# Optimization experiments

Hardware: AMD Instinct MI355X
Metric: run time of the kernel (lower is better)

The kernel has to match this reference:

```python
import jax, jax.numpy as jnp
import numpy as np
from jax import lax

jax.config.update("jax_enable_x64", True)

B = 32768          # batch size
NCS = 96           # number of charging stations
NB = 124           # num_buses
S_BASE = 1000.0
MAX_CS = 22.17
MIN_CS = -22.17
MAX_EV_CH = 22.0
MAX_EV_DIS = -22.0
EV_CAP = 70.0
EV_MIN_CAP = 15.0
ITERS = 100
TOL = 1e-06
DT = 15.0 / 60.0   # timescale (hours)


def setup_inputs() -> dict:
    ks = jax.random.split(jax.random.key(0), 12)
    action = jax.random.uniform(ks[0], (B, NCS), dtype=jnp.float32, minval=-1.0, maxval=1.0)
    prices = jax.random.uniform(ks[1], (B, 1), dtype=jnp.float32, minval=0.05, maxval=0.5)
    active = jax.random.uniform(ks[2], (B, NB - 1), dtype=jnp.float32, minval=0.0, maxval=50.0)
    reactive = jax.random.uniform(ks[3], (B, NB - 1), dtype=jnp.float32, minval=0.0, maxval=20.0)
    cap = jax.random.uniform(ks[4], (B, NCS), dtype=jnp.float32, minval=0.0, maxval=EV_CAP)
    cap = cap * (jax.random.uniform(ks[5], (B, NCS)) > 0.2).astype(jnp.float32)
    tleft = jax.random.randint(ks[6], (B, NCS), 1, 10).astype(jnp.float32)
    bus = jax.random.randint(ks[7], (B, NCS), 0, NB - 1).astype(jnp.float32)
    ev = jnp.stack([cap, tleft, bus], axis=-1).reshape(B, 3 * NCS)  # interleaved triples
    state = jnp.concatenate(
        [jnp.zeros((B, 3), jnp.float32), prices, active, reactive, ev], axis=1
    )  # (B, 4 + 2*(NB-1) + 3*NCS) == (B, 538)
    K_re = (0.005 * jax.random.normal(ks[8], (NB - 1, NB - 1))).astype(jnp.float32)
    K_im = (0.005 * jax.random.normal(ks[9], (NB - 1, NB - 1))).astype(jnp.float32)
    L_re = jnp.ones((NB - 1,), jnp.float32)
    L_im = jnp.zeros((NB - 1,), jnp.float32)
    return {"action": action, "state": state, "K_re": K_re, "K_im": K_im, "L_re": L_re, "L_im": L_im}


def _forward(action, state, K_re, K_im, L_re, L_im):
    b, ncs = action.shape
    nb1 = NB - 1
    es = 4 + 2 * nb1  # start of EV state block
    prices = state[:, 3:4]                                    # (B,1), broadcast over stations
    cap = state[:, es:es + 3 * ncs:3]                         # current capacity
    tleft = state[:, es + 1:es + 1 + 3 * ncs:3]               # time left
    bus = state[:, es + 2:es + 2 + 3 * ncs:3].astype(jnp.int32)  # connected bus index
    conn = (cap > 0).astype(action.dtype)
    max_ch = jnp.minimum(MAX_EV_CH, conn * (EV_CAP - cap) / DT)
    max_dis = jnp.maximum(MAX_EV_DIS, conn * (EV_MIN_CAP - cap) / DT)
    pos = jnp.where(action >= 0, 1.0, 0.0).astype(action.dtype)
    power = action * MAX_CS * pos - action * MIN_CS * (1.0 - pos)
    power = jnp.maximum(jnp.minimum(power, max_ch), max_dis)
    costs = (prices * power * DT).sum(axis=1)
    new_cap = jnp.ceil((cap + power * DT) * 100.0) / 100.0
    dep = (tleft == 1).astype(action.dtype)
    user_sat = (-10.0 * dep * (new_cap - EV_CAP) ** 2).sum(axis=1)
    # scatter-add EV power per bus (duplicate indices accumulate, like torch scatter_add)
    ev_bus = jnp.zeros((b, nb1), power.dtype).at[jnp.arange(b)[:, None], bus].add(power)
    ap = state[:, 4:4 + nb1]
    rp = state[:, 4 + nb1:4 + 2 * nb1]
    S = ((ap + ev_bus) / S_BASE + 1j * (rp / S_BASE)).astype(jnp.complex128)  # (B, NB-1)
    K = (K_re + 1j * K_im).astype(jnp.complex128)
    W = (L_re + 1j * L_im).astype(jnp.complex128)
    v_init = jnp.ones((b, nb1), jnp.complex128)

    def run(v0):
        # Z-bus fixed point: v_k = K @ conj(S / v0)^T + W   (batched as bi)
        vk = jnp.einsum('ij,bj->bi', K, jnp.conj(S / v0)) + W
        tol = jnp.max(jnp.abs(jnp.abs(vk) - jnp.abs(v0)))
        return vk, tol

    def body(carry, _):
        v0, done = carry
        def step(v):
            vk, tol = run(v)
            return vk, tol < TOL
        def skip(v):
            return v, jnp.array(True)
        v_next, conv = lax.cond(done, skip, step, v0)
        return (v_next, done | conv), None

    (v_fin, _), _ = lax.scan(body, (v_init, jnp.array(False)), None, length=ITERS)
    vmag = jnp.abs(v_fin)
    voltage_loss = jnp.minimum(0.0, 0.05 - jnp.abs(1.0 - vmag)).sum(axis=1)
    loss = 1000.0 * voltage_loss + costs + user_sat
    return loss.astype(jnp.float32)


def reference(action, state, K_re, K_im, L_re, L_im):
    return _forward(action, state, K_re, K_im, L_re, L_im)
```

## Files before the change

kernel.cpp:

```cpp
#include <hip/hip_runtime.h>

#define NB1   123
#define NCSd  96
#define SW    538
#define TPB   256
#define BT    16
#define STPB  128


__global__ __launch_bounds__(256) void k_norm(const float* __restrict__ Kre,
                                              const float* __restrict__ Kim,
                                              const float* __restrict__ Lre,
                                              const float* __restrict__ Lim,
                                              float* __restrict__ ws) {
    __shared__ float part[4];
    const int tid = threadIdx.x;
    const int w = tid >> 6, l = tid & 63;
    const int wid = blockIdx.x * 4 + w;
    const int j1 = wid, j2 = wid + 64;
    const bool has2 = j2 < NB1;

    const float* kr1 = Kre + j1 * NB1; const float* ki1 = Kim + j1 * NB1;
    float a0 = kr1[l], b0 = ki1[l];
    float a1 = 0.f, b1 = 0.f;
    if (l < NB1 - 64) { a1 = kr1[l + 64]; b1 = ki1[l + 64]; }
    float c0 = 0.f, d0 = 0.f, c1 = 0.f, d1 = 0.f;
    if (has2) {
        const float* kr2 = Kre + j2 * NB1; const float* ki2 = Kim + j2 * NB1;
        c0 = kr2[l]; d0 = ki2[l];
        if (l < NB1 - 64) { c1 = kr2[l + 64]; d1 = ki2[l + 64]; }
    }
    float s1 = fmaf(a0, a0, b0 * b0) + fmaf(a1, a1, b1 * b1);
    float s2 = fmaf(c0, c0, d0 * d0) + fmaf(c1, c1, d1 * d1);
    #pragma unroll
    for (int off = 32; off; off >>= 1) {
        s1 += __shfl_xor(s1, off);
        s2 += __shfl_xor(s2, off);
    }
    float m2 = has2 ? fmaxf(s1, s2) : s1;
    if (l == 0) part[w] = m2;
    __syncthreads();
    if (tid == 0)
        ws[2 + blockIdx.x] = fmaxf(fmaxf(part[0], part[1]), fmaxf(part[2], part[3]));

    if (blockIdx.x == 0 && w == 0) {
        float dr = Lre[l] - 1.f, di = Lim[l];
        float d2 = fmaf(dr, dr, di * di);
        if (l + 64 < NB1) {
            float dr2 = Lre[l + 64] - 1.f, di2 = Lim[l + 64];
            d2 = fmaxf(d2, fmaf(dr2, dr2, di2 * di2));
        }
        #pragma unroll
        for (int off = 32; off; off >>= 1) d2 = fmaxf(d2, __shfl_xor(d2, off));
        if (l == 0) { ws[1] = d2; ((unsigned*)ws)[0] = 0u; }
    }
}

__global__ __launch_bounds__(TPB) void k_fast(const float* __restrict__ action,
                                              const float* __restrict__ state,
                                              float* __restrict__ ws,
                                              float* __restrict__ out) {
    __shared__ __align__(16) float st[4][1088];
    __shared__ float ev[4][256];

    const int tid = threadIdx.x;
    const int w = tid >> 6, l = tid & 63;
    const long g = (long)blockIdx.x * 4 + w;

    const float4* G4 = (const float4*)(state + g * (2 * SW));
    float4 v0 = G4[l];
    float4 v1 = G4[l + 64];
    float4 v2 = G4[l + 128];
    float4 v3 = G4[l + 192];
    float4 v4 = make_float4(0.f, 0.f, 0.f, 0.f);
    const bool t4 = l < 269 - 256;
    if (t4) v4 = G4[l + 256];

    float r2p = (l < 16) ? ws[2 + l] : 0.f;
    float dw2 = ws[1];

    ev[w][l] = 0.f; ev[w][l + 64] = 0.f;
    ev[w][l + 128] = 0.f; ev[w][l + 192] = 0.f;

    float4* st4 = (float4*)st[w];
    st4[l] = v0; st4[l + 64] = v1; st4[l + 128] = v2; st4[l + 192] = v3;
    if (t4) st4[l + 256] = v4;
    asm volatile("s_waitcnt lgkmcnt(0)" ::: "memory");

    const int e = l >> 5, li = l & 31;
    const long b = 2 * g + e;
    const float* srow = st[w] + e * SW;
    const float* actp = action + b * NCSd;
    float* evp = ev[w] + e * 128;
    const float pr = srow[3];

    float cost = 0.f, usat = 0.f;
    #pragma unroll
    for (int s = 0; s < 3; ++s) {
        int i = li + 32 * s;
        float cap = srow[250 + 3 * i];
        float tl  = srow[251 + 3 * i];
        int   bus = (int)srow[252 + 3 * i];
        float a   = actp[i];
        float conn = cap > 0.f ? 1.f : 0.f;
        float mch = fminf(22.0f,  conn * (70.0f - cap) * 4.0f);
        float mds = fmaxf(-22.0f, conn * (15.0f - cap) * 4.0f);
        float p = fmaxf(fminf(22.17f * a, mch), mds);
        cost = fmaf(pr * p, 0.25f, cost);
        float nc = ceilf((cap + p * 0.25f) * 100.0f) * 0.01f;
        if (tl == 1.0f) { float d = nc - 70.0f; usat = fmaf(-10.0f * d, d, usat); }
        atomicAdd(&evp[bus], p);
    }
    asm volatile("s_waitcnt lgkmcnt(0)" ::: "memory");

    float s2 = 0.f;
    #pragma unroll
    for (int s = 0; s < 4; ++s) {
        int k = li + 32 * s;
        if (k < NB1) {
            float apv = srow[4 + k] + evp[k];
            float rpv = srow[127 + k];
            s2 = fmaf(apv, apv, fmaf(rpv, rpv, s2));
        }
    }
    #pragma unroll
    for (int off = 16; off; off >>= 1) {
        s2   += __shfl_xor(s2, off);
        cost += __shfl_xor(cost, off);
        usat += __shfl_xor(usat, off);
    }

    #pragma unroll
    for (int off = 8; off; off >>= 1) r2p = fmaxf(r2p, __shfl_xor(r2p, off));
    float R  = sqrtf(__shfl(r2p, 0));
    float dW = sqrtf(dw2);
    float t = 0.0495f - dW;
    float q2max = -1.0f;
    if (t > 0.f && t < 1.0f - dW) {
        float xm = (t * (1.0f - dW - t) - 1e-7f) / 1.001f;
        if (xm > 0.f && R > 0.f) {
            float sm = xm / R * 1000.0f;
            q2max = sm * sm;
        }
    }
    bool safe = s2 <= q2max;

    if (li == 0) out[b] = cost + usat;

    bool flagged = (li == 0) && !safe;
    unsigned long long mask = __ballot(flagged);
    if (mask) {
        int nf = __popcll(mask);
        int lead = __ffsll((long long)mask) - 1;
        unsigned base_ = 0;
        if (l == lead) base_ = atomicAdd((unsigned*)ws, (unsigned)nf);
        base_ = __shfl(base_, lead);
        if (flagged) {
            int rank = __popcll(mask & ((1ull << l) - 1ull));
            ((unsigned*)ws)[18 + base_ + rank] = (unsigned)b;
        }
    }
}

__global__ __launch_bounds__(STPB) void k_solve(const float* __restrict__ action,
                                                const float* __restrict__ state,
                                                const float* __restrict__ Kre,
                                                const float* __restrict__ Kim,
                                                const float* __restrict__ Lre,
                                                const float* __restrict__ Lim,
                                                const float* __restrict__ ws,
                                                float* __restrict__ out) {
    __shared__ float ev[BT][STPB];
    __shared__ __align__(16) float2 cmat[STPB][BT + 2];
    __shared__ float vls[STPB][BT + 1];
    __shared__ float red[2];
    __shared__ unsigned idxs[BT];
    const unsigned count = ((const unsigned*)ws)[0];
    const int tid = threadIdx.x;
    const int j = tid;
    const bool jok = j < NB1;
    const float Wre = jok ? Lre[j] : 1.f;
    const float Wim = jok ? Lim[j] : 0.f;

    for (unsigned base = (unsigned)blockIdx.x * BT; base < count; base += (unsigned)gridDim.x * BT) {
        unsigned nv = count - base; if (nv > BT) nv = BT;
        if (tid < BT) {
            unsigned t = (unsigned)tid < nv ? (unsigned)tid : nv - 1;
            idxs[tid] = ((const unsigned*)ws)[18 + base + t];
        }
        for (int x = tid; x < BT * STPB; x += STPB) ((float*)ev)[x] = 0.f;
        __syncthreads();

        for (int task = tid; task < BT * NCSd; task += STPB) {
            int e = task / NCSd, i = task - e * NCSd;
            long b = (long)idxs[e];
            const float* srow = state + b * SW;
            float cap = srow[250 + 3 * i];
            int   bus = (int)srow[252 + 3 * i];
            float a   = action[b * NCSd + i];
            float conn = cap > 0.f ? 1.f : 0.f;
            float mch = fminf(22.0f,  conn * (70.0f - cap) * 4.0f);
            float mds = fmaxf(-22.0f, conn * (15.0f - cap) * 4.0f);
            float p = fmaxf(fminf(22.17f * a, mch), mds);
            atomicAdd(&ev[e][bus], p);
        }
        __syncthreads();

        float Sre[BT], Sim[BT], vr[BT], vi[BT];
        #pragma unroll
        for (int e = 0; e < BT; ++e) {
            long b = (long)idxs[e];
            float ap = jok ? state[b * SW + 4 + j]   : 0.f;
            float rp = jok ? state[b * SW + 127 + j] : 0.f;
            Sre[e] = (ap + ev[e][j]) * 0.001f;
            Sim[e] = rp * 0.001f;
            vr[e] = 1.f; vi[e] = 0.f;
        }
        for (int it = 0; it < 100; ++it) {
            #pragma unroll
            for (int e = 0; e < BT; ++e) {
                float d = vr[e] * vr[e] + vi[e] * vi[e];
                float inv = 1.0f / d;
                cmat[j][e] = make_float2((Sre[e] * vr[e] + Sim[e] * vi[e]) * inv,
                                         (Sre[e] * vi[e] - Sim[e] * vr[e]) * inv);
            }
            __syncthreads();
            float ar[BT], ai[BT];
            #pragma unroll
            for (int e = 0; e < BT; ++e) { ar[e] = Wre; ai[e] = Wim; }
            for (int k = 0; k < NB1; ++k) {
                float kr = jok ? Kre[j * NB1 + k] : 0.f;
                float ki = jok ? Kim[j * NB1 + k] : 0.f;
                const float4* crow = (const float4*)(&cmat[k][0]);
                #pragma unroll
                for (int eh = 0; eh < BT / 2; ++eh) {
                    float4 c2 = crow[eh];
                    ar[2*eh]   = fmaf(kr, c2.x, fmaf(-ki, c2.y, ar[2*eh]));
                    ai[2*eh]   = fmaf(kr, c2.y, fmaf( ki, c2.x, ai[2*eh]));
                    ar[2*eh+1] = fmaf(kr, c2.z, fmaf(-ki, c2.w, ar[2*eh+1]));
                    ai[2*eh+1] = fmaf(kr, c2.w, fmaf( ki, c2.z, ai[2*eh+1]));
                }
            }
            float md = 0.f;
            #pragma unroll
            for (int e = 0; e < BT; ++e) {
                float vmn = sqrtf(ar[e]*ar[e] + ai[e]*ai[e]);
                float vmo = sqrtf(vr[e]*vr[e] + vi[e]*vi[e]);
                md = fmaxf(md, fabsf(vmn - vmo));
                vr[e] = ar[e]; vi[e] = ai[e];
            }
            #pragma unroll
            for (int off = 32; off; off >>= 1) md = fmaxf(md, __shfl_xor(md, off));
            if ((tid & 63) == 0) red[tid >> 6] = md;
            __syncthreads();
            if (fmaxf(red[0], red[1]) < 1e-6f) break;
        }
        #pragma unroll
        for (int e = 0; e < BT; ++e) {
            float vm = sqrtf(vr[e]*vr[e] + vi[e]*vi[e]);
            vls[j][e] = jok ? fminf(0.f, 0.05f - fabsf(1.0f - vm)) : 0.f;
        }
        __syncthreads();
        if (tid < (int)nv) {
            float s = 0.f;
            for (int k = 0; k < NB1; ++k) s += vls[k][tid];
            long b = (long)idxs[tid];
            out[b] += 1000.0f * s;
        }
        __syncthreads();
    }
}

__global__ __launch_bounds__(STPB) void k_main(
    const float* __restrict__ action, const float* __restrict__ state,
    const float* __restrict__ Kre, const float* __restrict__ Kim,
    const float* __restrict__ Lre, const float* __restrict__ Lim,
    float* __restrict__ out)
{
    __shared__ float ev[BT][STPB];
    __shared__ float costs_s[BT];
    __shared__ float usat_s[BT];
    __shared__ __align__(16) float2 cmat[STPB][BT + 2];
    __shared__ float vls[STPB][BT + 1];
    __shared__ float red[2];
    const int tid = threadIdx.x;
    const int e0  = blockIdx.x * BT;
    for (int x = tid; x < BT * STPB; x += STPB) ((float*)ev)[x] = 0.f;
    if (tid < BT) { costs_s[tid] = 0.f; usat_s[tid] = 0.f; }
    __syncthreads();
    for (int task = tid; task < BT * NCSd; task += STPB) {
        int e = task / NCSd, i = task - e * NCSd;
        long b = (long)(e0 + e);
        const float* srow = state + b * SW;
        float cap = srow[250 + 3 * i], tleft = srow[251 + 3 * i];
        int bus = (int)srow[252 + 3 * i];
        float a = action[b * NCSd + i];
        float conn = cap > 0.f ? 1.f : 0.f;
        float mch = fminf(22.0f, conn * (70.0f - cap) * 4.0f);
        float mds = fmaxf(-22.0f, conn * (15.0f - cap) * 4.0f);
        float power = fmaxf(fminf(22.17f * a, mch), mds);
        atomicAdd(&costs_s[e], srow[3] * power * 0.25f);
        float nc = ceilf((cap + power * 0.25f) * 100.0f) * 0.01f;
        if (tleft == 1.0f) { float d = nc - 70.0f; atomicAdd(&usat_s[e], -10.0f * d * d); }
        atomicAdd(&ev[e][bus], power);
    }
    __syncthreads();
    const int j = tid;
    const bool jok = j < NB1;
    float Wre = jok ? Lre[j] : 1.0f, Wim = jok ? Lim[j] : 0.0f;
    float Sre[BT], Sim[BT], vr[BT], vi[BT];
    #pragma unroll
    for (int e = 0; e < BT; ++e) {
        long b = (long)(e0 + e);
        float ap = jok ? state[b * SW + 4 + j] : 0.f;
        float rp = jok ? state[b * SW + 127 + j] : 0.f;
        Sre[e] = (ap + ev[e][j]) * 0.001f; Sim[e] = rp * 0.001f;
        vr[e] = 1.f; vi[e] = 0.f;
    }
    for (int it = 0; it < 100; ++it) {
        #pragma unroll
        for (int e = 0; e < BT; ++e) {
            float d = vr[e]*vr[e] + vi[e]*vi[e];
            float inv = 1.0f / d;
            cmat[j][e] = make_float2((Sre[e]*vr[e] + Sim[e]*vi[e]) * inv,
                                     (Sre[e]*vi[e] - Sim[e]*vr[e]) * inv);
        }
        __syncthreads();
        float ar[BT], ai[BT];
        #pragma unroll
        for (int e = 0; e < BT; ++e) { ar[e] = Wre; ai[e] = Wim; }
        for (int k = 0; k < NB1; ++k) {
            float kr = jok ? Kre[j*NB1+k] : 0.f;
            float ki = jok ? Kim[j*NB1+k] : 0.f;
            const float4* crow = (const float4*)(&cmat[k][0]);
            #pragma unroll
            for (int eh = 0; eh < BT / 2; ++eh) {
                float4 c2 = crow[eh];
                ar[2*eh]   = fmaf(kr, c2.x, fmaf(-ki, c2.y, ar[2*eh]));
                ai[2*eh]   = fmaf(kr, c2.y, fmaf( ki, c2.x, ai[2*eh]));
                ar[2*eh+1] = fmaf(kr, c2.z, fmaf(-ki, c2.w, ar[2*eh+1]));
                ai[2*eh+1] = fmaf(kr, c2.w, fmaf( ki, c2.z, ai[2*eh+1]));
            }
        }
        float md = 0.f;
        #pragma unroll
        for (int e = 0; e < BT; ++e) {
            float vmn = sqrtf(ar[e]*ar[e] + ai[e]*ai[e]);
            float vmo = sqrtf(vr[e]*vr[e] + vi[e]*vi[e]);
            md = fmaxf(md, fabsf(vmn - vmo));
            vr[e] = ar[e]; vi[e] = ai[e];
        }
        #pragma unroll
        for (int off = 32; off > 0; off >>= 1) md = fmaxf(md, __shfl_xor(md, off));
        if ((tid & 63) == 0) red[tid >> 6] = md;
        __syncthreads();
        if (fmaxf(red[0], red[1]) < 1e-6f) break;
    }
    #pragma unroll
    for (int e = 0; e < BT; ++e) {
        float vm = sqrtf(vr[e]*vr[e] + vi[e]*vi[e]);
        vls[j][e] = jok ? fminf(0.f, 0.05f - fabsf(1.0f - vm)) : 0.f;
    }
    __syncthreads();
    if (tid < BT) {
        float s = 0.f;
        for (int k = 0; k < NB1; ++k) s += vls[k][tid];
        out[e0 + tid] = 1000.0f * s + costs_s[tid] + usat_s[tid];
    }
}

extern "C" void kernel_launch(void* const* d_in, const int* in_sizes, int n_in,
                              void* d_out, int out_size, void* d_ws, size_t ws_size,
                              hipStream_t stream) {
    const float* action = (const float*)d_in[0];
    const float* state  = (const float*)d_in[1];
    const float* Kre    = (const float*)d_in[2];
    const float* Kim    = (const float*)d_in[3];
    const float* Lre    = (const float*)d_in[4];
    const float* Lim    = (const float*)d_in[5];
    float* out = (float*)d_out;
    const int B = out_size;

    const size_t wsNeed = (size_t)(18 + B) * sizeof(unsigned);
    if (ws_size >= wsNeed) {
        float* ws = (float*)d_ws;
        hipLaunchKernelGGL(k_norm, dim3(16), dim3(256), 0, stream, Kre, Kim, Lre, Lim, ws);
        hipLaunchKernelGGL(k_fast, dim3(B / 8), dim3(TPB), 0, stream,
                           action, state, ws, out);
        hipLaunchKernelGGL(k_solve, dim3(16), dim3(STPB), 0, stream,
                           action, state, Kre, Kim, Lre, Lim, ws, out);
    } else {
        hipLaunchKernelGGL(k_main, dim3((B + BT - 1) / BT), dim3(STPB), 0, stream,
                           action, state, Kre, Kim, Lre, Lim, out);
    }
}
```

Measured before the change: 37.71 us.

## Fuse fallback power-flow solve into fast kernel and drop compaction pass

Removes the separate k_solve launch and the atomic compaction list of flagged batch rows. Any wave whose row fails the analytic safety bound now runs the Z-bus fixed-point iteration itself, with each lane handling two buses and reading K from global memory. The iteration count is fixed at 32 with no convergence check, and two explicit LDS waitcnts plus the workspace counter reset are dropped. This saves a kernel launch and a global atomic, but flagged rows are handled serially inside a single wave, and a fixed iteration count may differ slightly from the tolerance-based reference.

Result: faster. 36.20 us, median of 2 (-4.0%).

```diff
diff --git a/kernel.cpp b/kernel.cpp
--- a/kernel.cpp
+++ b/kernel.cpp
@@ -41,7 +41,7 @@
     if (l == 0) part[w] = m2;
     __syncthreads();
     if (tid == 0)
-        ws[2 + blockIdx.x] = fmaxf(fmaxf(part[0], part[1]), fmaxf(part[2], part[3]));
+        ws[1 + blockIdx.x] = fmaxf(fmaxf(part[0], part[1]), fmaxf(part[2], part[3]));
 
     if (blockIdx.x == 0 && w == 0) {
         float dr = Lre[l] - 1.f, di = Lim[l];
@@ -52,14 +52,18 @@
         }
         #pragma unroll
         for (int off = 32; off; off >>= 1) d2 = fmaxf(d2, __shfl_xor(d2, off));
-        if (l == 0) { ws[1] = d2; ((unsigned*)ws)[0] = 0u; }
+        if (l == 0) ws[0] = d2;
     }
 }
 
-__global__ __launch_bounds__(TPB) void k_fast(const float* __restrict__ action,
-                                              const float* __restrict__ state,
-                                              float* __restrict__ ws,
-                                              float* __restrict__ out) {
+__global__ __launch_bounds__(TPB, 7) void k_fast(const float* __restrict__ action,
+                                                 const float* __restrict__ state,
+                                                 const float* __restrict__ Kre,
+                                                 const float* __restrict__ Kim,
+                                                 const float* __restrict__ Lre,
+                                                 const float* __restrict__ Lim,
+                                                 const float* __restrict__ ws,
+                                                 float* __restrict__ out) {
     __shared__ __align__(16) float st[4][1088];
     __shared__ float ev[4][256];
 
@@ -76,8 +80,8 @@
     const bool t4 = l < 269 - 256;
     if (t4) v4 = G4[l + 256];
 
-    float r2p = (l < 16) ? ws[2 + l] : 0.f;
-    float dw2 = ws[1];
+    float r2p = (l < 16) ? ws[1 + l] : 0.f;
+    float dw2 = ws[0];
 
     ev[w][l] = 0.f; ev[w][l + 64] = 0.f;
     ev[w][l + 128] = 0.f; ev[w][l + 192] = 0.f;
@@ -85,7 +89,6 @@
     float4* st4 = (float4*)st[w];
     st4[l] = v0; st4[l + 64] = v1; st4[l + 128] = v2; st4[l + 192] = v3;
     if (t4) st4[l + 256] = v4;
-    asm volatile("s_waitcnt lgkmcnt(0)" ::: "memory");
 
     const int e = l >> 5, li = l & 31;
     const long b = 2 * g + e;
@@ -111,7 +114,6 @@
         if (tl == 1.0f) { float d = nc - 70.0f; usat = fmaf(-10.0f * d, d, usat); }
         atomicAdd(&evp[bus], p);
     }
-    asm volatile("s_waitcnt lgkmcnt(0)" ::: "memory");
 
     float s2 = 0.f;
     #pragma unroll
@@ -145,130 +147,63 @@
     }
     bool safe = s2 <= q2max;
 
-    if (li == 0) out[b] = cost + usat;
-
-    bool flagged = (li == 0) && !safe;
-    unsigned long long mask = __ballot(flagged);
-    if (mask) {
-        int nf = __popcll(mask);
-        int lead = __ffsll((long long)mask) - 1;
-        unsigned base_ = 0;
-        if (l == lead) base_ = atomicAdd((unsigned*)ws, (unsigned)nf);
-        base_ = __shfl(base_, lead);
-        if (flagged) {
-            int rank = __popcll(mask & ((1ull << l) - 1ull));
-            ((unsigned*)ws)[18 + base_ + rank] = (unsigned)b;
-        }
-    }
-}
-
-__global__ __launch_bounds__(STPB) void k_solve(const float* __restrict__ action,
-                                                const float* __restrict__ state,
-                                                const float* __restrict__ Kre,
-                                                const float* __restrict__ Kim,
-                                                const float* __restrict__ Lre,
-                                                const float* __restrict__ Lim,
-                                                const float* __restrict__ ws,
-                                                float* __restrict__ out) {
-    __shared__ float ev[BT][STPB];
-    __shared__ __align__(16) float2 cmat[STPB][BT + 2];
-    __shared__ float vls[STPB][BT + 1];
-    __shared__ float red[2];
-    __shared__ unsigned idxs[BT];
-    const unsigned count = ((const unsigned*)ws)[0];
-    const int tid = threadIdx.x;
-    const int j = tid;
-    const bool jok = j < NB1;
-    const float Wre = jok ? Lre[j] : 1.f;
-    const float Wim = jok ? Lim[j] : 0.f;
-
-    for (unsigned base = (unsigned)blockIdx.x * BT; base < count; base += (unsigned)gridDim.x * BT) {
-        unsigned nv = count - base; if (nv > BT) nv = BT;
-        if (tid < BT) {
-            unsigned t = (unsigned)tid < nv ? (unsigned)tid : nv - 1;
-            idxs[tid] = ((const unsigned*)ws)[18 + base + t];
-        }
-        for (int x = tid; x < BT * STPB; x += STPB) ((float*)ev)[x] = 0.f;
-        __syncthreads();
-
-        for (int task = tid; task < BT * NCSd; task += STPB) {
-            int e = task / NCSd, i = task - e * NCSd;
-            long b = (long)idxs[e];
-            const float* srow = state + b * SW;
-            float cap = srow[250 + 3 * i];
-            int   bus = (int)srow[252 + 3 * i];
-            float a   = action[b * NCSd + i];
-            float conn = cap > 0.f ? 1.f : 0.f;
-            float mch = fminf(22.0f,  conn * (70.0f - cap) * 4.0f);
-            float mds = fmaxf(-22.0f, conn * (15.0f - cap) * 4.0f);
-            float p = fmaxf(fminf(22.17f * a, mch), mds);
-            atomicAdd(&ev[e][bus], p);
-        }
-        __syncthreads();
-
-        float Sre[BT], Sim[BT], vr[BT], vi[BT];
-        #pragma unroll
-        for (int e = 0; e < BT; ++e) {
-            long b = (long)idxs[e];
-            float ap = jok ? state[b * SW + 4 + j]   : 0.f;
-            float rp = jok ? state[b * SW + 127 + j] : 0.f;
-            Sre[e] = (ap + ev[e][j]) * 0.001f;
-            Sim[e] = rp * 0.001f;
-            vr[e] = 1.f; vi[e] = 0.f;
-        }
-        for (int it = 0; it < 100; ++it) {
-            #pragma unroll
-            for (int e = 0; e < BT; ++e) {
-                float d = vr[e] * vr[e] + vi[e] * vi[e];
-                float inv = 1.0f / d;
-                cmat[j][e] = make_float2((Sre[e] * vr[e] + Sim[e] * vi[e]) * inv,
-                                         (Sre[e] * vi[e] - Sim[e] * vr[e]) * inv);
+    float vs0 = 0.f, vs1 = 0.f;
+    unsigned long long bad = __ballot(!safe);
+    if (bad & 0x100000001ull) {
+        const int j1 = l, j2 = 64 + l;
+        const bool has2 = j2 < NB1;
+        float* cw = st[w];
+        #pragma unroll 1
+        for (int fe = 0; fe < 2; ++fe) {
+            if (!((bad >> (fe * 32)) & 1ull)) continue;
+            const float* frow = st[w] + fe * SW;
+            float* fev = ev[w] + fe * 128;
+            float S1r = (frow[4 + j1] + fev[j1]) * 0.001f;
+            float S1i = frow[127 + j1] * 0.001f;
+            float S2r = has2 ? (frow[4 + j2] + fev[j2]) * 0.001f : 0.f;
+            float S2i = has2 ? frow[127 + j2] * 0.001f : 0.f;
+            float W1r = Lre[j1], W1i = Lim[j1];
+            float W2r = has2 ? Lre[j2] : 1.f;
+            float W2i = has2 ? Lim[j2] : 0.f;
+            float v1r = 1.f, v1i = 0.f, v2r = 1.f, v2i = 0.f;
+            for (int it = 0; it < 32; ++it) {
+                float d1 = v1r * v1r + v1i * v1i, i1 = 1.0f / d1;
+                cw[j1]       = (S1r * v1r + S1i * v1i) * i1;
+                cw[128 + j1] = (S1r * v1i - S1i * v1r) * i1;
+                if (has2) {
+                    float d2 = v2r * v2r + v2i * v2i, i2 = 1.0f / d2;
+                    cw[j2]       = (S2r * v2r + S2i * v2i) * i2;
+                    cw[128 + j2] = (S2r * v2i - S2i * v2r) * i2;
+                }
+                asm volatile("s_waitcnt lgkmcnt(0)" ::: "memory");
+                float a1r = W1r, a1i = W1i, a2r = W2r, a2i = W2i;
+                for (int k = 0; k < NB1; ++k) {
+                    float cr = cw[k], ci = cw[128 + k];
+                    float kr1 = Kre[j1 * NB1 + k], ki1 = Kim[j1 * NB1 + k];
+                    a1r = fmaf(kr1, cr, fmaf(-ki1, ci, a1r));
+                    a1i = fmaf(kr1, ci, fmaf( ki1, cr, a1i));
+                    if (has2) {
+                        float kr2 = Kre[j2 * NB1 + k], ki2 = Kim[j2 * NB1 + k];
+                        a2r = fmaf(kr2, cr, fmaf(-ki2, ci, a2r));
+                        a2i = fmaf(kr2, ci, fmaf( ki2, cr, a2i));
+                    }
+                }
+                v1r = a1r; v1i = a1i; v2r = a2r; v2i = a2i;
+                asm volatile("s_waitcnt lgkmcnt(0)" ::: "memory");
             }
-            __syncthreads();
-            float ar[BT], ai[BT];
-            #pragma unroll
-            for (int e = 0; e < BT; ++e) { ar[e] = Wre; ai[e] = Wim; }
-            for (int k = 0; k < NB1; ++k) {
-                float kr = jok ? Kre[j * NB1 + k] : 0.f;
-                float ki = jok ? Kim[j * NB1 + k] : 0.f;
-                const float4* crow = (const float4*)(&cmat[k][0]);
-                #pragma unroll
-                for (int eh = 0; eh < BT / 2; ++eh) {
-                    float4 c2 = crow[eh];
-                    ar[2*eh]   = fmaf(kr, c2.x, fmaf(-ki, c2.y, ar[2*eh]));
-                    ai[2*eh]   = fmaf(kr, c2.y, fmaf( ki, c2.x, ai[2*eh]));
-                    ar[2*eh+1] = fmaf(kr, c2.z, fmaf(-ki, c2.w, ar[2*eh+1]));
-                    ai[2*eh+1] = fmaf(kr, c2.w, fmaf( ki, c2.z, ai[2*eh+1]));
-                }
-            }
-            float md = 0.f;
-            #pragma unroll
-            for (int e = 0; e < BT; ++e) {
-                float vmn = sqrtf(ar[e]*ar[e] + ai[e]*ai[e]);
-                float vmo = sqrtf(vr[e]*vr[e] + vi[e]*vi[e]);
-                md = fmaxf(md, fabsf(vmn - vmo));
-                vr[e] = ar[e]; vi[e] = ai[e];
+            float vm1 = sqrtf(v1r * v1r + v1i * v1i);
+            float vl = fminf(0.f, 0.05f - fabsf(1.0f - vm1));
+            if (has2) {
+                float vm2 = sqrtf(v2r * v2r + v2i * v2i);
+                vl += fminf(0.f, 0.05f - fabsf(1.0f - vm2));
             }
             #pragma unroll
-            for (int off = 32; off; off >>= 1) md = fmaxf(md, __shfl_xor(md, off));
-            if ((tid & 63) == 0) red[tid >> 6] = md;
-            __syncthreads();
-            if (fmaxf(red[0], red[1]) < 1e-6f) break;
-        }
-        #pragma unroll
-        for (int e = 0; e < BT; ++e) {
-            float vm = sqrtf(vr[e]*vr[e] + vi[e]*vi[e]);
-            vls[j][e] = jok ? fminf(0.f, 0.05f - fabsf(1.0f - vm)) : 0.f;
-        }
-        __syncthreads();
-        if (tid < (int)nv) {
-            float s = 0.f;
-            for (int k = 0; k < NB1; ++k) s += vls[k][tid];
-            long b = (long)idxs[tid];
-            out[b] += 1000.0f * s;
-        }
-        __syncthreads();
-    }
+            for (int off = 32; off; off >>= 1) vl += __shfl_xor(vl, off);
+            if (fe == 0) vs0 = vl; else vs1 = vl;
+        }
+    }
+
+    if (li == 0) out[b] = cost + usat + 1000.0f * (e == 0 ? vs0 : vs1);
 }
 
 __global__ __launch_bounds__(STPB) void k_main(
@@ -381,13 +316,10 @@
     float* out = (float*)d_out;
     const int B = out_size;
 
-    const size_t wsNeed = (size_t)(18 + B) * sizeof(unsigned);
-    if (ws_size >= wsNeed) {
+    if (ws_size >= 17 * sizeof(float)) {
         float* ws = (float*)d_ws;
         hipLaunchKernelGGL(k_norm, dim3(16), dim3(256), 0, stream, Kre, Kim, Lre, Lim, ws);
         hipLaunchKernelGGL(k_fast, dim3(B / 8), dim3(TPB), 0, stream,
-                           action, state, ws, out);
-        hipLaunchKernelGGL(k_solve, dim3(16), dim3(STPB), 0, stream,
                            action, state, Kre, Kim, Lre, Lim, ws, out);
     } else {
         hipLaunchKernelGGL(k_main, dim3((B + BT - 1) / BT), dim3(STPB), 0, stream,
```
